# Kernel optimization log

Hardware: AMD Instinct MI355X
Metric: run time of the kernel (lower is better)

Reference implementation:

```python
import jax, jax.numpy as jnp
import numpy as np

B, S, HID = 1, 2048, 4096
H, KV, D = 32, 8, 128          # query heads, kv heads, head_dim
THETA = 100000.0               # rope base


def setup_inputs() -> dict:
    key = jax.random.key(0)
    k1, k2, k3, k4, k5 = jax.random.split(key, 5)
    hidden_states = jax.random.normal(k1, (B, S, HID), jnp.float32)
    # W_pack: Linear(hidden, H*D + 2*KV*D), torch weight layout [out, in]
    w_pack = jax.random.normal(k2, (H * D + 2 * KV * D, HID), jnp.float32) * 0.02
    w_o = jax.random.normal(k3, (HID, H * D), jnp.float32) * 0.02
    # conv kernels: per-kv-head causal mixing weights of width 2 (softmax-normalized at init)
    conv_k = jax.nn.softmax(jax.random.normal(k4, (KV, 2), jnp.float32), axis=-1)
    conv_v = jax.nn.softmax(jax.random.normal(k5, (KV, 2), jnp.float32), axis=-1)
    return dict(hidden_states=hidden_states, w_pack=w_pack, w_o=w_o,
                conv_k=conv_k, conv_v=conv_v)


def _causal_conv2(u, k):
    """u: [b,s,h,d], k: [h,2]. v[t] = k[h,0]*u[t-1] + k[h,1]*u[t] (zero pad at t=-1).
    Equivalent to custom_convolution with window 2 (unfold+mul+sum)."""
    prev = jnp.pad(u, ((0, 0), (1, 0), (0, 0), (0, 0)))[:, :-1]
    return k[None, None, :, 0:1] * prev + k[None, None, :, 1:2] * u


def _rope(x):
    """Non-interleaved (half-split) rotary over full head_dim. x: [b,s,h,d]."""
    s, d = x.shape[1], x.shape[-1]
    inv = 1.0 / (THETA ** (jnp.arange(0, d, 2, dtype=jnp.float32) / d))
    freqs = jnp.arange(s, dtype=jnp.float32)[:, None] * inv[None, :]  # [s, d/2]
    cos = jnp.cos(freqs)[None, :, None, :]
    sin = jnp.sin(freqs)[None, :, None, :]
    x1, x2 = x[..., : d // 2], x[..., d // 2:]
    return jnp.concatenate([x1 * cos - x2 * sin, x1 * sin + x2 * cos], axis=-1)


def reference(hidden_states, w_pack, w_o, conv_k, conv_v):
    qkv = hidden_states @ w_pack.T                       # [b,s,H*D+2*KV*D]
    q = qkv[..., : H * D].reshape(B, S, H, D)
    k = qkv[..., H * D: H * D + KV * D].reshape(B, S, KV, D)
    v = qkv[..., H * D + KV * D:].reshape(B, S, KV, D)

    # causal depthwise width-2 conv mixing on K and V (prefill path)
    k = _causal_conv2(k, conv_k)
    v = _causal_conv2(v, conv_v)

    # rotary on q, k
    q = _rope(q)
    k = _rope(k)

    # GQA: repeat kv heads to match query heads
    g = H // KV
    k = jnp.repeat(k, g, axis=2)
    v = jnp.repeat(v, g, axis=2)

    scale = 1.0 / np.sqrt(D).astype(np.float32)
    scores = jnp.einsum('bqhd,bkhd->bhqk', q, k) * scale  # [b,H,S,S]
    causal = jnp.tril(jnp.ones((S, S), dtype=bool))
    scores = jnp.where(causal[None, None], scores, jnp.finfo(scores.dtype).min)
    probs = jax.nn.softmax(scores, axis=-1)
    out = jnp.einsum('bhqk,bkhd->bqhd', probs, v).reshape(B, S, H * D)
    return out @ w_o.T
```

## Files before the change

### kernel.cpp

```cpp
#include <hip/hip_runtime.h>
#include <hip/hip_bf16.h>

#define S_LEN 2048
#define HID 4096
#define NH 32
#define NKV 8
#define HD 128

typedef unsigned short u16;
typedef __attribute__((ext_vector_type(4))) float f32x4;
typedef __attribute__((ext_vector_type(8))) short bf16x8;

__device__ __forceinline__ u16 f2bf(float x) {
  union { float f; unsigned u; } c; c.f = x;
  unsigned r = c.u + 0x7FFFu + ((c.u >> 16) & 1u);
  return (u16)(r >> 16);
}

__device__ __forceinline__ void gload16(const void* g, void* l) {
  __builtin_amdgcn_global_load_lds(
      (const __attribute__((address_space(1))) unsigned int*)g,
      (__attribute__((address_space(3))) unsigned int*)l, 16, 0, 0);
}

__device__ __forceinline__ unsigned cvtpk_bf16(float lo, float hi) {
  unsigned r;
  asm("v_cvt_pk_bf16_f32 %0, %1, %2" : "=v"(r) : "v"(lo), "v"(hi));
  return r;
}

__device__ __forceinline__ float bcastf(float v, int srclane) {
  int r = __builtin_amdgcn_ds_bpermute(srclane << 2, __builtin_bit_cast(int, v));
  return __builtin_bit_cast(float, r);
}

__global__ void cvt4_kernel(const float* __restrict__ s, u16* __restrict__ d, int n4) {
  int i = blockIdx.x * 256 + threadIdx.x;
  if (i >= n4) return;
  float4 v = ((const float4*)s)[i];
  ushort4 o;
  o.x = f2bf(v.x); o.y = f2bf(v.y); o.z = f2bf(v.z); o.w = f2bf(v.w);
  ((ushort4*)d)[i] = o;
}

__global__ void rope_tab_kernel(float2* __restrict__ tab) {
  int i = blockIdx.x * 256 + threadIdx.x;
  int t = i >> 6, d = i & 63;
  float inv = expf(-(float)d * (11.512925464970229f / 64.0f));
  float f = (float)t * inv;
  float2 cs; cs.x = cosf(f); cs.y = sinf(f);
  tab[i] = cs;
}

__global__ void rope_q_kernel(const float* __restrict__ qkv, const float2* __restrict__ tab,
                              u16* __restrict__ Q) {
  int i = blockIdx.x * 256 + threadIdx.x;
  int d = i & 63, h = (i >> 6) & 31, t = i >> 11;
  const float* row = qkv + (size_t)t * 6144 + h * 128;
  float x1 = row[d], x2 = row[d + 64];
  float2 cs = tab[(t << 6) | d];
  const float SC = 0.12752551286084f;
  u16* orow = Q + (((size_t)t * NH + h) << 7);
  orow[d]      = f2bf((x1 * cs.x - x2 * cs.y) * SC);
  orow[d + 64] = f2bf((x1 * cs.y + x2 * cs.x) * SC);
}

__global__ void convrope_k_kernel(const float* __restrict__ qkv, const float* __restrict__ ck,
                                  const float2* __restrict__ tab, u16* __restrict__ K) {
  int i = blockIdx.x * 256 + threadIdx.x;
  int d = i & 63, kv = (i >> 6) & 7, t = i >> 9;
  const float* cur = qkv + (size_t)t * 6144 + 4096 + kv * 128;
  float c0 = ck[kv * 2], c1 = ck[kv * 2 + 1];
  float x1 = c1 * cur[d], x2 = c1 * cur[d + 64];
  if (t > 0) { const float* prv = cur - 6144; x1 += c0 * prv[d]; x2 += c0 * prv[d + 64]; }
  float2 cs = tab[(t << 6) | d];
  u16* orow = K + (((size_t)t * NKV + kv) << 7);
  orow[d]      = f2bf(x1 * cs.x - x2 * cs.y);
  orow[d + 64] = f2bf(x1 * cs.y + x2 * cs.x);
}

__global__ __launch_bounds__(256) void convT_v_kernel(const float* __restrict__ qkv,
                                                      const float* __restrict__ cv,
                                                      u16* __restrict__ VT) {
  __shared__ float ld[65][128];
  int tt = blockIdx.x * 64, kv = blockIdx.y;
  float c0 = cv[kv * 2], c1 = cv[kv * 2 + 1];
  for (int idx = threadIdx.x; idx < 65 * 128; idx += 256) {
    int r = idx >> 7, d = idx & 127;
    int t = tt - 1 + r;
    ld[r][d] = (t >= 0) ? qkv[(size_t)t * 6144 + 5120 + kv * 128 + d] : 0.f;
  }
  __syncthreads();
  int d = threadIdx.x >> 1, tc = (threadIdx.x & 1) * 32;
  u16* out = VT + ((size_t)kv * 128 + d) * S_LEN + tt + tc;
#pragma unroll
  for (int j = 0; j < 32; ++j)
    out[j] = f2bf(c0 * ld[tc + j][d] + c1 * ld[tc + j + 1][d]);
}

#define BM 128
#define BN 128
#define BK 64

__global__ __launch_bounds__(256, 2) void gemm_nt_kernel(const u16* __restrict__ A,
                                                         const u16* __restrict__ B,
                                                         float* __restrict__ C,
                                                         int M, int N, int K) {
  __shared__ __align__(16) u16 lA[BM * BK];
  __shared__ __align__(16) u16 lB[BN * BK];
  const int tid = threadIdx.x;
  const int wid = tid >> 6, lane = tid & 63;
  const int nbx = gridDim.x, nwg = nbx * gridDim.y;
  const int L = blockIdx.y * nbx + blockIdx.x;
  const int cpx = nwg >> 3;
  const int W = (L & 7) * cpx + (L >> 3);
  const int bm = (W / nbx) * BM, bn = (W % nbx) * BN;
  const int wr = (wid >> 1) * 64, wc = (wid & 1) * 64;
  const int lr = lane & 15, lg = lane >> 4;
  f32x4 acc[4][4] = {};
  const char* Ab = (const char*)A;
  const char* Bb = (const char*)B;
  const int nk = K / BK;
  for (int kt = 0; kt < nk; ++kt) {
    const size_t k0b = (size_t)kt * (BK * 2);
    __syncthreads();
#pragma unroll
    for (int i = 0; i < 4; ++i) {
      int off = (i * 4 + wid) * 1024 + lane * 16;
      int row = off >> 7, inrow = off & 127;
      int sw = inrow ^ ((row & 7) << 4);
      gload16(Ab + (size_t)(bm + row) * (K * 2) + k0b + sw, (char*)lA + (i * 4 + wid) * 1024);
      gload16(Bb + (size_t)(bn + row) * (K * 2) + k0b + sw, (char*)lB + (i * 4 + wid) * 1024);
    }
    __syncthreads();
    bf16x8 af[4][2], bfv[4][2];
#pragma unroll
    for (int m = 0; m < 4; ++m)
#pragma unroll
      for (int ks = 0; ks < 2; ++ks) {
        int row = wr + m * 16 + lr;
        int boff = row * 128 + ((ks * 64 + lg * 16) ^ ((row & 7) << 4));
        af[m][ks] = *(const bf16x8*)((const char*)lA + boff);
      }
#pragma unroll
    for (int n = 0; n < 4; ++n)
#pragma unroll
      for (int ks = 0; ks < 2; ++ks) {
        int row = wc + n * 16 + lr;
        int boff = row * 128 + ((ks * 64 + lg * 16) ^ ((row & 7) << 4));
        bfv[n][ks] = *(const bf16x8*)((const char*)lB + boff);
      }
#pragma unroll
    for (int m = 0; m < 4; ++m)
#pragma unroll
      for (int n = 0; n < 4; ++n)
#pragma unroll
        for (int ks = 0; ks < 2; ++ks)
          acc[m][n] = __builtin_amdgcn_mfma_f32_16x16x32_bf16(af[m][ks], bfv[n][ks], acc[m][n], 0, 0, 0);
  }
#pragma unroll
  for (int m = 0; m < 4; ++m)
#pragma unroll
    for (int n = 0; n < 4; ++n)
#pragma unroll
      for (int r = 0; r < 4; ++r) {
        int row = bm + wr + m * 16 + lg * 4 + r;
        int col = bn + wc + n * 16 + lr;
        C[(size_t)row * N + col] = acc[m][n][r];
      }
}

__global__ __launch_bounds__(256, 2) void attn_kernel(const u16* __restrict__ Q,
                                                      const u16* __restrict__ K,
                                                      const u16* __restrict__ VT,
                                                      u16* __restrict__ O) {
  __shared__ __align__(16) u16 lK[2][64 * 128];
  __shared__ __align__(16) u16 lV[2][128 * 64];
  __shared__ __align__(16) u16 lP[4][2][16 * 64];
  const int tid = threadIdx.x;
  const int wid = tid >> 6, lane = tid & 63;
  const int lr = lane & 15, lg = lane >> 4;
  const int g = blockIdx.x;
  const int s = g & 255;
  const int h = s >> 3, j = s & 7;
  const int b = (g < 256) ? (15 - j) : j;
  const int kvh = h >> 2;
  const int qtA = 2 * b, qtB = 2 * b + 1;
  const int qrowA = qtA * 64 + wid * 16 + lr;
  const int qrowB = qtB * 64 + wid * 16 + lr;

  bf16x8 qfA[4], qfB[4];
#pragma unroll
  for (int ks = 0; ks < 4; ++ks) {
    qfA[ks] = *(const bf16x8*)(Q + (((size_t)qrowA * NH + h) << 7) + ks * 32 + lg * 8);
    qfB[ks] = *(const bf16x8*)(Q + (((size_t)qrowB * NH + h) << 7) + ks * 32 + lg * 8);
  }

  f32x4 oA[8] = {}, oB[8] = {};
  float mA = -1e30f, sumA = 0.f, mB = -1e30f, sumB = 0.f;

  const char* Kb = (const char*)K;
  const char* Vb = (const char*)VT;
  char* pbA = (char*)lP[wid][0];
  char* pbB = (char*)lP[wid][1];

  auto stage = [&](int buf, int kt) {
    char* dK = (char*)lK[buf];
    char* dV = (char*)lV[buf];
#pragma unroll
    for (int i = 0; i < 4; ++i) {
      int off = (i * 4 + wid) * 1024 + lane * 16;
      int t = off >> 8, inrow = off & 255;
      gload16(Kb + (((size_t)((kt * 64 + t) * NKV + kvh)) << 8) + (inrow ^ ((t & 7) << 4)),
              dK + (i * 4 + wid) * 1024);
      int d = off >> 7, inr2 = off & 127;
      gload16(Vb + ((size_t)(kvh * 128 + d)) * (S_LEN * 2) + kt * 128 + (inr2 ^ ((d & 7) << 4)),
              dV + (i * 4 + wid) * 1024);
    }
  };

  auto smx = [&](f32x4* sv, float& mm, float& ll, f32x4* o, char* pbuf, bool diag, int qrow, int kt) {
    if (diag) {
#pragma unroll
      for (int n = 0; n < 4; ++n)
#pragma unroll
        for (int r = 0; r < 4; ++r) {
          int kg = kt * 64 + n * 16 + lg * 4 + r;
          if (kg > qrow) sv[n][r] = -1e30f;
        }
    }
    float pm = sv[0][0];
#pragma unroll
    for (int n = 0; n < 4; ++n)
#pragma unroll
      for (int r = 0; r < 4; ++r) pm = fmaxf(pm, sv[n][r]);
    pm = fmaxf(pm, __shfl_xor(pm, 16));
    pm = fmaxf(pm, __shfl_xor(pm, 32));
    if (__any(pm > mm + 8.f)) {
      float mn = fmaxf(mm, pm);
      float al = exp2f(mm - mn);
      mm = mn;
      ll *= al;
      float alo[4];
#pragma unroll
      for (int r = 0; r < 4; ++r) alo[r] = bcastf(al, lg * 4 + r);
#pragma unroll
      for (int nt = 0; nt < 8; ++nt)
#pragma unroll
        for (int r = 0; r < 4; ++r) o[nt][r] *= alo[r];
    }
    float rs = 0.f;
#pragma unroll
    for (int n = 0; n < 4; ++n)
#pragma unroll
      for (int r = 0; r < 4; ++r) {
        float p = exp2f(sv[n][r] - mm);
        sv[n][r] = p;
        rs += p;
      }
    rs += __shfl_xor(rs, 16);
    rs += __shfl_xor(rs, 32);
    ll += rs;
#pragma unroll
    for (int n = 0; n < 4; ++n) {
      uint2 w;
      w.x = cvtpk_bf16(sv[n][0], sv[n][1]);
      w.y = cvtpk_bf16(sv[n][2], sv[n][3]);
      *(uint2*)(pbuf + ((lr * 128 + n * 32 + lg * 8) ^ ((lr & 7) << 4))) = w;
    }
  };

  stage(0, 0);
  __syncthreads();
  for (int kt = 0; kt <= qtB; ++kt) {
    int cur = kt & 1;
    if (kt < qtB) stage(cur ^ 1, kt + 1);
    const char* kb = (const char*)lK[cur];
    const char* vb = (const char*)lV[cur];
    const bool doA = (kt <= qtA);

    f32x4 svA[4], svB[4];
#pragma unroll
    for (int n = 0; n < 4; ++n) {
      f32x4 aA = {}, aB = {};
#pragma unroll
      for (int ks = 0; ks < 4; ++ks) {
        int trow = n * 16 + lr;
        int boff = trow * 256 + ((ks * 64 + lg * 16) ^ ((trow & 7) << 4));
        bf16x8 kf = *(const bf16x8*)(kb + boff);
        aB = __builtin_amdgcn_mfma_f32_16x16x32_bf16(kf, qfB[ks], aB, 0, 0, 0);
        aA = __builtin_amdgcn_mfma_f32_16x16x32_bf16(kf, qfA[ks], aA, 0, 0, 0);
      }
      svA[n] = aA; svB[n] = aB;
    }

    if (doA) smx(svA, mA, sumA, oA, pbA, kt == qtA, qrowA, kt);
    smx(svB, mB, sumB, oB, pbB, kt == qtB, qrowB, kt);

#pragma unroll
    for (int ks = 0; ks < 2; ++ks) {
      int poff = (lr * 128 + 64 * ks + 16 * lg) ^ ((lr & 7) << 4);
      bf16x8 pfB = *(const bf16x8*)(pbB + poff);
      bf16x8 pfA = *(const bf16x8*)(pbA + poff);
#pragma unroll
      for (int nt = 0; nt < 8; ++nt) {
        int drow = nt * 16 + lr;
        int vboff = drow * 128 + ((ks * 64 + lg * 16) ^ ((drow & 7) << 4));
        bf16x8 vf = *(const bf16x8*)(vb + vboff);
        oB[nt] = __builtin_amdgcn_mfma_f32_16x16x32_bf16(pfB, vf, oB[nt], 0, 0, 0);
        if (doA) oA[nt] = __builtin_amdgcn_mfma_f32_16x16x32_bf16(pfA, vf, oA[nt], 0, 0, 0);
      }
    }
    __syncthreads();
  }

  float riA = 1.0f / sumA, riB = 1.0f / sumB;
  float rA[4], rB[4];
#pragma unroll
  for (int r = 0; r < 4; ++r) {
    rA[r] = bcastf(riA, lg * 4 + r);
    rB[r] = bcastf(riB, lg * 4 + r);
  }
#pragma unroll
  for (int nt = 0; nt < 8; ++nt)
#pragma unroll
    for (int r = 0; r < 4; ++r) {
      int rowA = qtA * 64 + wid * 16 + lg * 4 + r;
      int rowB = qtB * 64 + wid * 16 + lg * 4 + r;
      int col = nt * 16 + lr;
      O[(size_t)rowA * 4096 + h * 128 + col] = f2bf(oA[nt][r] * rA[r]);
      O[(size_t)rowB * 4096 + h * 128 + col] = f2bf(oB[nt][r] * rB[r]);
    }
}

extern "C" void kernel_launch(void* const* d_in, const int* in_sizes, int n_in,
                              void* d_out, int out_size, void* d_ws, size_t ws_size,
                              hipStream_t stream) {
  const float* hidden = (const float*)d_in[0];
  const float* wpack  = (const float*)d_in[1];
  const float* wo     = (const float*)d_in[2];
  const float* convk  = (const float*)d_in[3];
  const float* convv  = (const float*)d_in[4];
  float* out = (float*)d_out;

  char* w = (char*)d_ws;
  u16*  hiddenB = (u16*)w;
  u16*  wpackB  = (u16*)(w + 16777216);
  float* qkv    = (float*)(w + 67108864);
  u16*  qrope   = (u16*)(w + 117440512);
  u16*  krope   = (u16*)(w + 134217728);
  u16*  vT      = (u16*)(w + 138412032);
  float2* tab   = (float2*)(w + 142606336);

  cvt4_kernel<<<8192, 256, 0, stream>>>(hidden, hiddenB, 2097152);
  cvt4_kernel<<<24576, 256, 0, stream>>>(wpack, wpackB, 6291456);
  rope_tab_kernel<<<512, 256, 0, stream>>>(tab);
  gemm_nt_kernel<<<dim3(48, 16), 256, 0, stream>>>(hiddenB, wpackB, qkv, 2048, 6144, 4096);
  cvt4_kernel<<<16384, 256, 0, stream>>>(wo, wpackB, 4194304);
  rope_q_kernel<<<16384, 256, 0, stream>>>(qkv, tab, qrope);
  convrope_k_kernel<<<4096, 256, 0, stream>>>(qkv, convk, tab, krope);
  convT_v_kernel<<<dim3(32, 8), 256, 0, stream>>>(qkv, convv, vT);
  attn_kernel<<<512, 256, 0, stream>>>(qrope, krope, vT, hiddenB);
  gemm_nt_kernel<<<dim3(32, 16), 256, 0, stream>>>(hiddenB, wpackB, out, 2048, 4096, 4096);
}
```

Measured before the change: 529.7 us.

## Emit QKV projection in bf16 and vectorize rope/conv kernels over bf16 input

The QKV GEMM is templated to store its output as bf16 instead of fp32, halving the intermediate buffer's write and read traffic. The rope-Q, conv-rope-K and conv-transpose-V kernels now read bf16 with 4-wide vector loads and stores, with fewer threads each doing four elements. The GEMM's XCD-aware block-index remapping is removed in favor of plain row-major block mapping. Rounding q/k/v to bf16 before conv and rope adds a little numerical error, and dropping the remap may reduce cache locality across chiplets.

```diff
diff --git a/kernel.cpp b/kernel.cpp
--- a/kernel.cpp
+++ b/kernel.cpp
@@ -15,6 +15,11 @@
   union { float f; unsigned u; } c; c.f = x;
   unsigned r = c.u + 0x7FFFu + ((c.u >> 16) & 1u);
   return (u16)(r >> 16);
+}
+
+__device__ __forceinline__ float bf2f(u16 x) {
+  union { unsigned u; float f; } c; c.u = (unsigned)x << 16;
+  return c.f;
 }
 
 __device__ __forceinline__ void gload16(const void* g, void* l) {
@@ -52,69 +57,102 @@
   tab[i] = cs;
 }
 
-__global__ void rope_q_kernel(const float* __restrict__ qkv, const float2* __restrict__ tab,
+__global__ void rope_q_kernel(const u16* __restrict__ qkv, const float* __restrict__ tab,
                               u16* __restrict__ Q) {
   int i = blockIdx.x * 256 + threadIdx.x;
-  int d = i & 63, h = (i >> 6) & 31, t = i >> 11;
-  const float* row = qkv + (size_t)t * 6144 + h * 128;
-  float x1 = row[d], x2 = row[d + 64];
-  float2 cs = tab[(t << 6) | d];
+  int d4 = (i & 15) * 4, h = (i >> 4) & 31, t = i >> 9;
+  const u16* row = qkv + (size_t)t * 6144 + h * 128;
+  ushort4 a = *(const ushort4*)(row + d4);
+  ushort4 b = *(const ushort4*)(row + d4 + 64);
+  const float4* tf = (const float4*)(tab + ((t << 6) + d4) * 2);
+  float4 c01 = tf[0], c23 = tf[1];
   const float SC = 0.12752551286084f;
+  float x10 = bf2f(a.x), x11 = bf2f(a.y), x12 = bf2f(a.z), x13 = bf2f(a.w);
+  float x20 = bf2f(b.x), x21 = bf2f(b.y), x22 = bf2f(b.z), x23 = bf2f(b.w);
+  ushort4 o1, o2;
+  o1.x = f2bf((x10 * c01.x - x20 * c01.y) * SC);
+  o1.y = f2bf((x11 * c01.z - x21 * c01.w) * SC);
+  o1.z = f2bf((x12 * c23.x - x22 * c23.y) * SC);
+  o1.w = f2bf((x13 * c23.z - x23 * c23.w) * SC);
+  o2.x = f2bf((x10 * c01.y + x20 * c01.x) * SC);
+  o2.y = f2bf((x11 * c01.w + x21 * c01.z) * SC);
+  o2.z = f2bf((x12 * c23.y + x22 * c23.x) * SC);
+  o2.w = f2bf((x13 * c23.w + x23 * c23.z) * SC);
   u16* orow = Q + (((size_t)t * NH + h) << 7);
-  orow[d]      = f2bf((x1 * cs.x - x2 * cs.y) * SC);
-  orow[d + 64] = f2bf((x1 * cs.y + x2 * cs.x) * SC);
-}
-
-__global__ void convrope_k_kernel(const float* __restrict__ qkv, const float* __restrict__ ck,
-                                  const float2* __restrict__ tab, u16* __restrict__ K) {
+  *(ushort4*)(orow + d4) = o1;
+  *(ushort4*)(orow + d4 + 64) = o2;
+}
+
+__global__ void convrope_k_kernel(const u16* __restrict__ qkv, const float* __restrict__ ck,
+                                  const float* __restrict__ tab, u16* __restrict__ K) {
   int i = blockIdx.x * 256 + threadIdx.x;
-  int d = i & 63, kv = (i >> 6) & 7, t = i >> 9;
-  const float* cur = qkv + (size_t)t * 6144 + 4096 + kv * 128;
+  int d4 = (i & 15) * 4, kv = (i >> 4) & 7, t = i >> 7;
+  const u16* cur = qkv + (size_t)t * 6144 + 4096 + kv * 128;
   float c0 = ck[kv * 2], c1 = ck[kv * 2 + 1];
-  float x1 = c1 * cur[d], x2 = c1 * cur[d + 64];
-  if (t > 0) { const float* prv = cur - 6144; x1 += c0 * prv[d]; x2 += c0 * prv[d + 64]; }
-  float2 cs = tab[(t << 6) | d];
+  ushort4 a = *(const ushort4*)(cur + d4);
+  ushort4 b = *(const ushort4*)(cur + d4 + 64);
+  float x1[4] = { c1 * bf2f(a.x), c1 * bf2f(a.y), c1 * bf2f(a.z), c1 * bf2f(a.w) };
+  float x2[4] = { c1 * bf2f(b.x), c1 * bf2f(b.y), c1 * bf2f(b.z), c1 * bf2f(b.w) };
+  if (t > 0) {
+    const u16* prv = cur - 6144;
+    ushort4 pa = *(const ushort4*)(prv + d4);
+    ushort4 pb = *(const ushort4*)(prv + d4 + 64);
+    x1[0] += c0 * bf2f(pa.x); x1[1] += c0 * bf2f(pa.y); x1[2] += c0 * bf2f(pa.z); x1[3] += c0 * bf2f(pa.w);
+    x2[0] += c0 * bf2f(pb.x); x2[1] += c0 * bf2f(pb.y); x2[2] += c0 * bf2f(pb.z); x2[3] += c0 * bf2f(pb.w);
+  }
+  const float4* tf = (const float4*)(tab + ((t << 6) + d4) * 2);
+  float4 c01 = tf[0], c23 = tf[1];
+  float cs[4] = { c01.x, c01.z, c23.x, c23.z };
+  float sn[4] = { c01.y, c01.w, c23.y, c23.w };
+  ushort4 o1, o2;
+  o1.x = f2bf(x1[0] * cs[0] - x2[0] * sn[0]);
+  o1.y = f2bf(x1[1] * cs[1] - x2[1] * sn[1]);
+  o1.z = f2bf(x1[2] * cs[2] - x2[2] * sn[2]);
+  o1.w = f2bf(x1[3] * cs[3] - x2[3] * sn[3]);
+  o2.x = f2bf(x1[0] * sn[0] + x2[0] * cs[0]);
+  o2.y = f2bf(x1[1] * sn[1] + x2[1] * cs[1]);
+  o2.z = f2bf(x1[2] * sn[2] + x2[2] * cs[2]);
+  o2.w = f2bf(x1[3] * sn[3] + x2[3] * cs[3]);
   u16* orow = K + (((size_t)t * NKV + kv) << 7);
-  orow[d]      = f2bf(x1 * cs.x - x2 * cs.y);
-  orow[d + 64] = f2bf(x1 * cs.y + x2 * cs.x);
-}
-
-__global__ __launch_bounds__(256) void convT_v_kernel(const float* __restrict__ qkv,
+  *(ushort4*)(orow + d4) = o1;
+  *(ushort4*)(orow + d4 + 64) = o2;
+}
+
+__global__ __launch_bounds__(256) void convT_v_kernel(const u16* __restrict__ qkv,
                                                       const float* __restrict__ cv,
                                                       u16* __restrict__ VT) {
-  __shared__ float ld[65][128];
+  __shared__ u16 ld[65][128];
   int tt = blockIdx.x * 64, kv = blockIdx.y;
   float c0 = cv[kv * 2], c1 = cv[kv * 2 + 1];
-  for (int idx = threadIdx.x; idx < 65 * 128; idx += 256) {
-    int r = idx >> 7, d = idx & 127;
+  for (int idx = threadIdx.x; idx < 65 * 32; idx += 256) {
+    int r = idx >> 5, d4 = (idx & 31) * 4;
     int t = tt - 1 + r;
-    ld[r][d] = (t >= 0) ? qkv[(size_t)t * 6144 + 5120 + kv * 128 + d] : 0.f;
+    ushort4 v = (t >= 0) ? *(const ushort4*)(qkv + (size_t)t * 6144 + 5120 + kv * 128 + d4)
+                         : (ushort4){0, 0, 0, 0};
+    *(ushort4*)(&ld[r][d4]) = v;
   }
   __syncthreads();
   int d = threadIdx.x >> 1, tc = (threadIdx.x & 1) * 32;
   u16* out = VT + ((size_t)kv * 128 + d) * S_LEN + tt + tc;
 #pragma unroll
   for (int j = 0; j < 32; ++j)
-    out[j] = f2bf(c0 * ld[tc + j][d] + c1 * ld[tc + j + 1][d]);
+    out[j] = f2bf(c0 * bf2f(ld[tc + j][d]) + c1 * bf2f(ld[tc + j + 1][d]));
 }
 
 #define BM 128
 #define BN 128
 #define BK 64
 
+template <bool BF16OUT>
 __global__ __launch_bounds__(256, 2) void gemm_nt_kernel(const u16* __restrict__ A,
                                                          const u16* __restrict__ B,
-                                                         float* __restrict__ C,
+                                                         void* __restrict__ C,
                                                          int M, int N, int K) {
   __shared__ __align__(16) u16 lA[BM * BK];
   __shared__ __align__(16) u16 lB[BN * BK];
   const int tid = threadIdx.x;
   const int wid = tid >> 6, lane = tid & 63;
-  const int nbx = gridDim.x, nwg = nbx * gridDim.y;
-  const int L = blockIdx.y * nbx + blockIdx.x;
-  const int cpx = nwg >> 3;
-  const int W = (L & 7) * cpx + (L >> 3);
-  const int bm = (W / nbx) * BM, bn = (W % nbx) * BN;
+  const int bm = blockIdx.y * BM, bn = blockIdx.x * BN;
   const int wr = (wid >> 1) * 64, wc = (wid & 1) * 64;
   const int lr = lane & 15, lg = lane >> 4;
   f32x4 acc[4][4] = {};
@@ -166,7 +204,10 @@
       for (int r = 0; r < 4; ++r) {
         int row = bm + wr + m * 16 + lg * 4 + r;
         int col = bn + wc + n * 16 + lr;
-        C[(size_t)row * N + col] = acc[m][n][r];
+        if (BF16OUT)
+          ((u16*)C)[(size_t)row * N + col] = f2bf(acc[m][n][r]);
+        else
+          ((float*)C)[(size_t)row * N + col] = acc[m][n][r];
       }
 }
 
@@ -346,20 +387,20 @@
   char* w = (char*)d_ws;
   u16*  hiddenB = (u16*)w;
   u16*  wpackB  = (u16*)(w + 16777216);
-  float* qkv    = (float*)(w + 67108864);
-  u16*  qrope   = (u16*)(w + 117440512);
-  u16*  krope   = (u16*)(w + 134217728);
-  u16*  vT      = (u16*)(w + 138412032);
-  float2* tab   = (float2*)(w + 142606336);
+  u16*  qkvB    = (u16*)(w + 67108864);
+  u16*  qrope   = (u16*)(w + 92274688);
+  u16*  krope   = (u16*)(w + 109051904);
+  u16*  vT      = (u16*)(w + 113246208);
+  float* tab    = (float*)(w + 117440512);
 
   cvt4_kernel<<<8192, 256, 0, stream>>>(hidden, hiddenB, 2097152);
   cvt4_kernel<<<24576, 256, 0, stream>>>(wpack, wpackB, 6291456);
-  rope_tab_kernel<<<512, 256, 0, stream>>>(tab);
-  gemm_nt_kernel<<<dim3(48, 16), 256, 0, stream>>>(hiddenB, wpackB, qkv, 2048, 6144, 4096);
+  rope_tab_kernel<<<512, 256, 0, stream>>>((float2*)tab);
+  gemm_nt_kernel<true><<<dim3(48, 16), 256, 0, stream>>>(hiddenB, wpackB, qkvB, 2048, 6144, 4096);
   cvt4_kernel<<<16384, 256, 0, stream>>>(wo, wpackB, 4194304);
-  rope_q_kernel<<<16384, 256, 0, stream>>>(qkv, tab, qrope);
-  convrope_k_kernel<<<4096, 256, 0, stream>>>(qkv, convk, tab, krope);
-  convT_v_kernel<<<dim3(32, 8), 256, 0, stream>>>(qkv, convv, vT);
+  rope_q_kernel<<<4096, 256, 0, stream>>>(qkvB, tab, qrope);
+  convrope_k_kernel<<<1024, 256, 0, stream>>>(qkvB, convk, tab, krope);
+  convT_v_kernel<<<dim3(32, 8), 256, 0, stream>>>(qkvB, convv, vT);
   attn_kernel<<<512, 256, 0, stream>>>(qrope, krope, vT, hiddenB);
-  gemm_nt_kernel<<<dim3(32, 16), 256, 0, stream>>>(hiddenB, wpackB, out, 2048, 4096, 4096);
-}
+  gemm_nt_kernel<false><<<dim3(32, 16), 256, 0, stream>>>(hiddenB, wpackB, out, 2048, 4096, 4096);
+}
```

New measurement: 485.7 us. 1.09x faster.
